# Kernel optimization log

Measured on AMD Instinct MI355X. Metric: run time of the kernel, lower is better.

Reference implementation:

```python
import jax, jax.numpy as jnp
import numpy as np

EPS = 0.1
TANH_SCALE = 1.0
B, T, N, D, C, DE = 8, 120, 24, 48, 1128, 256  # C = D*(D-1)//2


def setup_inputs() -> dict:
    key = jax.random.key(0)
    k1, k2, k3, k4 = jax.random.split(key, 4)
    x = jax.random.normal(k1, (B, T, N, D), dtype=jnp.float32)
    context = jax.random.normal(k2, (B, C, N, DE), dtype=jnp.float32)
    Wkv = jax.random.normal(k3, (D, DE), dtype=jnp.float32) * (DE ** -0.5)
    bkv = jax.random.normal(k4, (D,), dtype=jnp.float32) * 0.01
    return {"x": x, "context": context, "Wkv": Wkv, "bkv": bkv}


def reference(x, context, Wkv, bkv):
    # x: [B,T,N,D], context: [B,C,N,DE]
    b, t, n, d = x.shape
    kv = jnp.einsum('bcne,de->bcnd', context, Wkv) + bkv      # [B,C,N,D]
    kv = jnp.transpose(kv, (0, 2, 3, 1))                      # [B,N,D,C]
    xt = jnp.transpose(x, (0, 2, 1, 3))                       # [B,N,T,D]
    sp = jnp.einsum('bntd,bndc->bntc', xt, kv)                # [B,N,T,C]
    sp = EPS * TANH_SCALE * jnp.tanh(sp / TANH_SCALE)
    i, j = jnp.tril_indices(d, k=-1)
    A = jnp.zeros((b, n, t, d, d), dtype=x.dtype).at[..., i, j].set(sp)
    A = A - jnp.swapaxes(A, -1, -2)                           # skew-symmetric
    dx = jnp.einsum('bntd,bntde->bnte', xt, A)                # per-(B,N,T) matvec
    y = xt + dx
    return jnp.transpose(y, (0, 2, 1, 3))                     # [B,T,N,D]
```

## Files before the change

### kernel.cpp

```cpp
#include <hip/hip_runtime.h>
#include <hip/hip_bf16.h>


constexpr int Bc = 8, Tc = 120, Nc = 24, Dc = 48, Cc = 1128, DEc = 256;
constexpr int BNc = Bc * Nc;
constexpr int KVP = 64;

using short8 = __attribute__((ext_vector_type(8))) short;
using f32x4  = __attribute__((ext_vector_type(4))) float;

__device__ __forceinline__ ushort f2b(float f) {
    union { float f; unsigned u; } v; v.f = f;
    unsigned r = (v.u + 0x7fffu + ((v.u >> 16) & 1u)) >> 16;
    return (ushort)r;
}
__device__ __forceinline__ float b2f(ushort u) {
    union { unsigned q; float f; } cv; cv.q = ((unsigned)u) << 16; return cv.f;
}
__device__ __forceinline__ short bcast(float f) {
    return (short)__bfloat16_as_ushort(__float2bfloat16(f));
}
__device__ __forceinline__ short8 pack8(const float4& a, const float4& b) {
    short8 r;
    r[0] = bcast(a.x); r[1] = bcast(a.y); r[2] = bcast(a.z); r[3] = bcast(a.w);
    r[4] = bcast(b.x); r[5] = bcast(b.y); r[6] = bcast(b.z); r[7] = bcast(b.w);
    return r;
}

__global__ void k0w(const float* __restrict__ Wkv, ushort* __restrict__ wkvb) {
    int i = blockIdx.x * 256 + threadIdx.x;
    float4 w = *reinterpret_cast<const float4*>(Wkv + i * 4);
    ushort4 u;
    u.x = (ushort)bcast(w.x); u.y = (ushort)bcast(w.y);
    u.z = (ushort)bcast(w.z); u.w = (ushort)bcast(w.w);
    *reinterpret_cast<ushort4*>(wkvb + i * 4) = u;
}

constexpr int SWs = 264;
__global__ __launch_bounds__(256) void k1_kv(const float* __restrict__ ctx,
                                             const ushort* __restrict__ wkvb,
                                             const float* __restrict__ bkv,
                                             ushort* __restrict__ kvb) {
    __shared__ ushort sW[Dc * SWs];
    const int bn = blockIdx.x, c0 = blockIdx.y * 128;
    const int b = bn / Nc, n = bn % Nc;
    const int tid = threadIdx.x, wave = tid >> 6, lane = tid & 63;
    const int tr = lane & 15, kg = lane >> 4;
    const float* ctxb = ctx + ((size_t)b * Cc * Nc + n) * DEc;

    for (int l = tid; l < Dc * 32; l += 256) {
        int d = l >> 5, e = (l & 31) << 3;
        *reinterpret_cast<short8*>(&sW[d * SWs + e]) =
            *reinterpret_cast<const short8*>(&wkvb[d * DEc + e]);
    }

    const float* crow[2];
    #pragma unroll
    for (int cn = 0; cn < 2; ++cn) {
        int c = c0 + wave * 32 + cn * 16 + tr;
        crow[cn] = ctxb + (size_t)(c < Cc ? c : Cc - 1) * (Nc * DEc);
    }

    f32x4 acc[3][2];
    #pragma unroll
    for (int mf = 0; mf < 3; ++mf)
        #pragma unroll
        for (int cn = 0; cn < 2; ++cn) acc[mf][cn] = (f32x4){0.f, 0.f, 0.f, 0.f};

    __syncthreads();

    #pragma unroll
    for (int ks = 0; ks < 8; ++ks) {
        const int e0 = ks * 32 + kg * 8;
        short8 bfrag[2];
        #pragma unroll
        for (int cn = 0; cn < 2; ++cn) {
            float4 a0 = *reinterpret_cast<const float4*>(crow[cn] + e0);
            float4 a1 = *reinterpret_cast<const float4*>(crow[cn] + e0 + 4);
            bfrag[cn] = pack8(a0, a1);
        }
        short8 afrag[3];
        #pragma unroll
        for (int mf = 0; mf < 3; ++mf)
            afrag[mf] = *reinterpret_cast<const short8*>(&sW[(mf * 16 + tr) * SWs + e0]);
        #pragma unroll
        for (int mf = 0; mf < 3; ++mf)
            #pragma unroll
            for (int cn = 0; cn < 2; ++cn)
                acc[mf][cn] = __builtin_amdgcn_mfma_f32_16x16x32_bf16(afrag[mf], bfrag[cn], acc[mf][cn], 0, 0, 0);
    }

    float4 bias[3];
    #pragma unroll
    for (int mf = 0; mf < 3; ++mf)
        bias[mf] = *reinterpret_cast<const float4*>(bkv + mf * 16 + kg * 4);
    #pragma unroll
    for (int cn = 0; cn < 2; ++cn) {
        int c = c0 + wave * 32 + cn * 16 + tr;
        if (c < Cc) {
            ushort* dst = kvb + ((size_t)bn * Cc + c) * KVP;
            #pragma unroll
            for (int mf = 0; mf < 3; ++mf) {
                ushort4 u;
                u.x = f2b(acc[mf][cn][0] + bias[mf].x);
                u.y = f2b(acc[mf][cn][1] + bias[mf].y);
                u.z = f2b(acc[mf][cn][2] + bias[mf].z);
                u.w = f2b(acc[mf][cn][3] + bias[mf].w);
                *reinterpret_cast<ushort4*>(dst + mf * 16 + kg * 4) = u;
            }
        }
    }
    {
        int row = lane >> 1, half = lane & 1;
        int c = c0 + wave * 32 + row;
        if (c < Cc) {
            short8 z = (short8){0, 0, 0, 0, 0, 0, 0, 0};
            *reinterpret_cast<short8*>(&kvb[((size_t)bn * Cc + c) * KVP + 48 + half * 8]) = z;
        }
    }
}

constexpr int SG2 = 1140;
__global__ __launch_bounds__(256, 3) void k2_fused(const float* __restrict__ x,
                                                   const ushort* __restrict__ kvb,
                                                   float* __restrict__ out) {
    __shared__ ushort sG[16 * SG2];
    __shared__ float  sXf[16 * 52];
    __shared__ ushort sXb[16 * 72];
    const int L = blockIdx.x;
    const int bn = (L & 7) + 8 * (L >> 6);
    const int tt = (L >> 3) & 7;
    const int b = bn / Nc, n = bn % Nc, t0 = tt * 16;
    const int tid = threadIdx.x, wave = tid >> 6, lane = tid & 63;
    const int tr = lane & 15, kg = lane >> 4;

    for (int l = tid; l < 16 * 72 / 4; l += 256)
        *reinterpret_cast<ushort4*>(&sXb[l * 4]) = make_ushort4(0, 0, 0, 0);
    for (int l = tid; l < 16 * 12; l += 256)
        sG[(l / 12) * SG2 + 1128 + (l % 12)] = 0;
    __syncthreads();
    if (tid < 192) {
        int t = tid / 12, dv = (tid % 12) * 4, tg = t0 + t;
        float4 v = make_float4(0.f, 0.f, 0.f, 0.f);
        if (tg < Tc) v = *reinterpret_cast<const float4*>(x + (((size_t)b * Tc + tg) * Nc + n) * Dc + dv);
        *reinterpret_cast<float4*>(&sXf[t * 52 + dv]) = v;
        *reinterpret_cast<ushort4*>(&sXb[t * 72 + dv]) = make_ushort4(f2b(v.x), f2b(v.y), f2b(v.z), f2b(v.w));
    }
    __syncthreads();
    const short8 af0 = *reinterpret_cast<const short8*>(&sXb[tr * 72 + kg * 8]);
    const short8 af1 = *reinterpret_cast<const short8*>(&sXb[tr * 72 + 32 + kg * 8]);

    const ushort* kvbn = kvb + (size_t)bn * Cc * KVP;
    short8 b0, b1, p0, p1;
    {
        int c = wave * 16 + tr;
        const ushort* p = kvbn + (size_t)c * KVP + kg * 8;
        b0 = *reinterpret_cast<const short8*>(p);
        b1 = *reinterpret_cast<const short8*>(p + 32);
    }
    #pragma unroll
    for (int u = 0; u < 18; ++u) {
        if (u < 17) {
            int c = (wave + (u + 1) * 4) * 16 + tr; if (c > Cc - 1) c = Cc - 1;
            const ushort* p = kvbn + (size_t)c * KVP + kg * 8;
            p0 = *reinterpret_cast<const short8*>(p);
            p1 = *reinterpret_cast<const short8*>(p + 32);
        }
        f32x4 a = (f32x4){0.f, 0.f, 0.f, 0.f};
        a = __builtin_amdgcn_mfma_f32_16x16x32_bf16(af0, b0, a, 0, 0, 0);
        a = __builtin_amdgcn_mfma_f32_16x16x32_bf16(af1, b1, a, 0, 0, 0);
        int c = (wave + u * 4) * 16 + tr;
        if (c < Cc) {
            #pragma unroll
            for (int r = 0; r < 4; ++r) {
                float g = 0.1f - 0.2f * __builtin_amdgcn_rcpf(__expf(2.0f * a[r]) + 1.0f);
                sG[(kg * 4 + r) * SG2 + c] = f2b(g);
            }
        }
        b0 = p0; b1 = p1;
    }
    __syncthreads();

    int ea[3], ta[3], tea[3];
    float dxa[3];
    #pragma unroll
    for (int p = 0; p < 3; ++p) {
        int idx = tid + p * 256;
        ta[p] = idx / 48; ea[p] = idx % 48;
        tea[p] = ea[p] * (ea[p] - 1) / 2;
        dxa[p] = 0.f;
    }
    int td = 0;
    #pragma unroll 4
    for (int d = 0; d < 48; ++d) {
        #pragma unroll
        for (int p = 0; p < 3; ++p) {
            bool gt = d > ea[p];
            int c = gt ? (td + ea[p]) : (tea[p] + d);
            float gv = b2f(sG[ta[p] * SG2 + c]);
            float xv = sXf[ta[p] * 52 + d];
            float m = gt ? xv : -xv;
            if (d == ea[p]) m = 0.f;
            dxa[p] = fmaf(m, gv, dxa[p]);
        }
        td += d;
    }
    #pragma unroll
    for (int p = 0; p < 3; ++p) {
        int tg = t0 + ta[p];
        if (tg < Tc)
            out[(((size_t)b * Tc + tg) * Nc + n) * Dc + ea[p]] = sXf[ta[p] * 52 + ea[p]] + dxa[p];
    }
}

extern "C" void kernel_launch(void* const* d_in, const int* in_sizes, int n_in,
                              void* d_out, int out_size, void* d_ws, size_t ws_size,
                              hipStream_t stream) {
    (void)in_sizes; (void)n_in; (void)out_size; (void)ws_size;
    const float* x   = (const float*)d_in[0];
    const float* ctx = (const float*)d_in[1];
    const float* Wkv = (const float*)d_in[2];
    const float* bkv = (const float*)d_in[3];
    float* out   = (float*)d_out;
    ushort* wkvb = (ushort*)d_ws;
    ushort* kvb  = (ushort*)((char*)d_ws + 32768);

    k0w<<<dim3(12), dim3(256), 0, stream>>>(Wkv, wkvb);
    k1_kv<<<dim3(BNc, 9), dim3(256), 0, stream>>>(ctx, wkvb, bkv, kvb);
    k2_fused<<<dim3(BNc * 8), dim3(256), 0, stream>>>(x, kvb, out);
}
```

Before: 94.22 us.

## Build x MFMA fragments from global, deepen kv prefetch, raise occupancy

```diff
diff --git a/kernel.cpp b/kernel.cpp
--- a/kernel.cpp
+++ b/kernel.cpp
@@ -121,12 +121,11 @@
 }
 
 constexpr int SG2 = 1140;
-__global__ __launch_bounds__(256, 3) void k2_fused(const float* __restrict__ x,
+__global__ __launch_bounds__(256, 4) void k2_fused(const float* __restrict__ x,
                                                    const ushort* __restrict__ kvb,
                                                    float* __restrict__ out) {
     __shared__ ushort sG[16 * SG2];
     __shared__ float  sXf[16 * 52];
-    __shared__ ushort sXb[16 * 72];
     const int L = blockIdx.x;
     const int bn = (L & 7) + 8 * (L >> 6);
     const int tt = (L >> 3) & 7;
@@ -134,41 +133,50 @@
     const int tid = threadIdx.x, wave = tid >> 6, lane = tid & 63;
     const int tr = lane & 15, kg = lane >> 4;
 
-    for (int l = tid; l < 16 * 72 / 4; l += 256)
-        *reinterpret_cast<ushort4*>(&sXb[l * 4]) = make_ushort4(0, 0, 0, 0);
     for (int l = tid; l < 16 * 12; l += 256)
         sG[(l / 12) * SG2 + 1128 + (l % 12)] = 0;
-    __syncthreads();
     if (tid < 192) {
         int t = tid / 12, dv = (tid % 12) * 4, tg = t0 + t;
         float4 v = make_float4(0.f, 0.f, 0.f, 0.f);
         if (tg < Tc) v = *reinterpret_cast<const float4*>(x + (((size_t)b * Tc + tg) * Nc + n) * Dc + dv);
         *reinterpret_cast<float4*>(&sXf[t * 52 + dv]) = v;
-        *reinterpret_cast<ushort4*>(&sXb[t * 72 + dv]) = make_ushort4(f2b(v.x), f2b(v.y), f2b(v.z), f2b(v.w));
-    }
-    __syncthreads();
-    const short8 af0 = *reinterpret_cast<const short8*>(&sXb[tr * 72 + kg * 8]);
-    const short8 af1 = *reinterpret_cast<const short8*>(&sXb[tr * 72 + 32 + kg * 8]);
+    }
+    short8 af0, af1;
+    {
+        int tg = t0 + tr; if (tg > Tc - 1) tg = Tc - 1;
+        const float* xrow = x + (((size_t)b * Tc + tg) * Nc + n) * Dc;
+        float4 a0 = *reinterpret_cast<const float4*>(xrow + kg * 8);
+        float4 a1 = *reinterpret_cast<const float4*>(xrow + kg * 8 + 4);
+        af0 = pack8(a0, a1);
+        if (kg < 2) {
+            float4 c0v = *reinterpret_cast<const float4*>(xrow + 32 + kg * 8);
+            float4 c1v = *reinterpret_cast<const float4*>(xrow + 32 + kg * 8 + 4);
+            af1 = pack8(c0v, c1v);
+        } else af1 = (short8){0, 0, 0, 0, 0, 0, 0, 0};
+    }
 
     const ushort* kvbn = kvb + (size_t)bn * Cc * KVP;
-    short8 b0, b1, p0, p1;
-    {
-        int c = wave * 16 + tr;
+    short8 R0[3], R1[3];
+    #pragma unroll
+    for (int s = 0; s < 2; ++s) {
+        int c = (wave + s * 4) * 16 + tr;
         const ushort* p = kvbn + (size_t)c * KVP + kg * 8;
-        b0 = *reinterpret_cast<const short8*>(p);
-        b1 = *reinterpret_cast<const short8*>(p + 32);
+        R0[s] = *reinterpret_cast<const short8*>(p);
+        R1[s] = *reinterpret_cast<const short8*>(p + 32);
     }
     #pragma unroll
     for (int u = 0; u < 18; ++u) {
-        if (u < 17) {
-            int c = (wave + (u + 1) * 4) * 16 + tr; if (c > Cc - 1) c = Cc - 1;
+        const int cur = u % 3;
+        f32x4 a = (f32x4){0.f, 0.f, 0.f, 0.f};
+        a = __builtin_amdgcn_mfma_f32_16x16x32_bf16(af0, R0[cur], a, 0, 0, 0);
+        a = __builtin_amdgcn_mfma_f32_16x16x32_bf16(af1, R1[cur], a, 0, 0, 0);
+        if (u + 2 < 18) {
+            const int nxt = (u + 2) % 3;
+            int c = (wave + (u + 2) * 4) * 16 + tr; if (c > Cc - 1) c = Cc - 1;
             const ushort* p = kvbn + (size_t)c * KVP + kg * 8;
-            p0 = *reinterpret_cast<const short8*>(p);
-            p1 = *reinterpret_cast<const short8*>(p + 32);
-        }
-        f32x4 a = (f32x4){0.f, 0.f, 0.f, 0.f};
-        a = __builtin_amdgcn_mfma_f32_16x16x32_bf16(af0, b0, a, 0, 0, 0);
-        a = __builtin_amdgcn_mfma_f32_16x16x32_bf16(af1, b1, a, 0, 0, 0);
+            R0[nxt] = *reinterpret_cast<const short8*>(p);
+            R1[nxt] = *reinterpret_cast<const short8*>(p + 32);
+        }
         int c = (wave + u * 4) * 16 + tr;
         if (c < Cc) {
             #pragma unroll
@@ -177,7 +185,6 @@
                 sG[(kg * 4 + r) * SG2 + c] = f2b(g);
             }
         }
-        b0 = p0; b1 = p1;
     }
     __syncthreads();
 
```

Result: no change. 94.77 us (+0.6%).
